# Kernel tuning notes

Measured on AMD Instinct MI355X. Metric: run time of the kernel, lower is better.

The kernel has to match this reference:

```python
import jax, jax.numpy as jnp
import numpy as np

R = 131072          # total proposals (ROIs)
D = 1024            # input feature dim (ShapeSpec.channels)
NUM_CLASSES = 80    # COCO foreground classes
REID_DIM = 256      # reid_feat_dim
BOX_DIM = 4


def setup_inputs() -> dict:
    key = jax.random.key(0)
    ks = jax.random.split(key, 12)
    x = jax.random.normal(ks[0], (R, D), dtype=jnp.float32)
    # cls_score: Linear(D, num_classes+1), init std=0.01, bias 0
    W_cls = 0.01 * jax.random.normal(ks[1], (NUM_CLASSES + 1, D), dtype=jnp.float32)
    b_cls = jnp.zeros((NUM_CLASSES + 1,), dtype=jnp.float32)
    # bbox_pred: Linear(D, num_classes * 4), init std=0.001, bias 0
    W_bbox = 0.001 * jax.random.normal(ks[2], (NUM_CLASSES * BOX_DIM, D), dtype=jnp.float32)
    b_bbox = jnp.zeros((NUM_CLASSES * BOX_DIM,), dtype=jnp.float32)
    # reid_embed_head: MLP(D, 256, 256, 3) -> Linear(D,256), Linear(256,256), Linear(256,256)
    def lin(k, fan_in, fan_out):
        kw, kb = jax.random.split(k)
        bound = 1.0 / np.sqrt(fan_in)
        W = jax.random.uniform(kw, (fan_out, fan_in), minval=-bound, maxval=bound, dtype=jnp.float32)
        b = jax.random.uniform(kb, (fan_out,), minval=-bound, maxval=bound, dtype=jnp.float32)
        return W, b
    W1, b1 = lin(ks[3], D, REID_DIM)
    W2, b2 = lin(ks[4], REID_DIM, REID_DIM)
    W3, b3 = lin(ks[5], REID_DIM, REID_DIM)
    return {"x": x, "W_cls": W_cls, "b_cls": b_cls, "W_bbox": W_bbox, "b_bbox": b_bbox,
            "W1": W1, "b1": b1, "W2": W2, "b2": b2, "W3": W3, "b3": b3}


def reference(x, W_cls, b_cls, W_bbox, b_bbox, W1, b1, W2, b2, W3, b3):
    # x: [R, D] (already flat; torch forward flattens if dim > 2)
    scores = x @ W_cls.T + b_cls                 # [R, K+1]
    proposal_deltas = x @ W_bbox.T + b_bbox      # [R, K*4]
    # MLP with ReLU on all but last layer
    h = jax.nn.relu(x @ W1.T + b1)               # [R, 256]
    h = jax.nn.relu(h @ W2.T + b2)               # [R, 256]
    embeds = h @ W3.T + b3                       # [R, 256]
    return scores, proposal_deltas, embeds
```

## Files before the change

### kernel.cpp

```cpp
#include <hip/hip_runtime.h>
#include <hip/hip_bf16.h>
#include <stdint.h>

#define R_TOT   131072
#define D_IN    1024
#define N_CLS   81
#define N_BOX   320
#define N_H     256
#define N1_USED 657
#define N1_PAD  768
#define NB_COLS 256

typedef __attribute__((ext_vector_type(8))) short short8;
typedef __attribute__((ext_vector_type(4))) float f32x4;

__device__ __forceinline__ unsigned short f2bf(float f) {
  union { float f; unsigned u; } v; v.f = f;
  unsigned r = v.u + 0x7FFFu + ((v.u >> 16) & 1u);
  return (unsigned short)(r >> 16);
}

__device__ __forceinline__ short8 cvt8(float4 a, float4 b) {
  short8 v;
  v[0] = (short)f2bf(a.x); v[1] = (short)f2bf(a.y);
  v[2] = (short)f2bf(a.z); v[3] = (short)f2bf(a.w);
  v[4] = (short)f2bf(b.x); v[5] = (short)f2bf(b.y);
  v[6] = (short)f2bf(b.z); v[7] = (short)f2bf(b.w);
  return v;
}

__device__ __forceinline__ void async_lds16(void* lds, const void* g) {
  __builtin_amdgcn_global_load_lds(
      (const __attribute__((address_space(1))) unsigned int*)g,
      (__attribute__((address_space(3))) unsigned int*)lds, 16, 0, 0);
}

__global__ void prep_w1(const float* __restrict__ Wc, const float* __restrict__ Wb,
                        const float* __restrict__ W1, unsigned short* __restrict__ Wp)
{
  int idx = blockIdx.x * 256 + threadIdx.x;
  int p   = idx / (N1_PAD * 32);
  int rem = idx % (N1_PAD * 32);
  int n   = rem >> 5;
  int kk  = rem & 31;
  int k   = p * 32 + kk;
  float w = 0.f;
  if (n < N_CLS)               w = Wc[(size_t)n * D_IN + k];
  else if (n < N_CLS + N_BOX)  w = Wb[(size_t)(n - N_CLS) * D_IN + k];
  else if (n < N1_USED)        w = W1[(size_t)(n - (N_CLS + N_BOX)) * D_IN + k];
  Wp[idx] = f2bf(w);
}

__global__ void prep_w23(const float* __restrict__ W2, const float* __restrict__ W3,
                         unsigned short* __restrict__ W2b, unsigned short* __restrict__ W3b)
{
  int idx = blockIdx.x * 256 + threadIdx.x;
  if (idx < 65536) W2b[idx] = f2bf(W2[idx]);
  else             W3b[idx - 65536] = f2bf(W3[idx - 65536]);
}

__global__ __launch_bounds__(512) void g1_kernel(
    const float* __restrict__ x, const unsigned short* __restrict__ Wp,
    const float* __restrict__ b_cls, const float* __restrict__ b_box,
    const float* __restrict__ b1,
    float* __restrict__ scores, float* __restrict__ deltas,
    unsigned short* __restrict__ h1)
{
  __shared__ __attribute__((aligned(16))) unsigned short As[64 * 256];

  const int tid  = threadIdx.x;
  const int wave = tid >> 6;
  const int lane = tid & 63;
  const int orig  = blockIdx.x;
  const int work  = (orig & 7) * 768 + (orig >> 3);
  const int m0    = (work / 3) * 64;
  const int nbase = (work % 3) * NB_COLS;

  const int lr  = lane & 15;
  const int hig = lane >> 4;
  const int g2  = hig * 8;

  f32x4 acc[4][2];
#pragma unroll
  for (int i = 0; i < 4; ++i)
#pragma unroll
    for (int j = 0; j < 2; ++j)
      acc[i][j] = (f32x4){0.f, 0.f, 0.f, 0.f};

  const unsigned short* bptr = Wp + (size_t)(nbase + wave * 32 + lr) * 32 + g2;
  const size_t BSTEP = (size_t)N1_PAD * 32;

  short8 bCur0 = *(const short8*)(bptr);
  short8 bCur1 = *(const short8*)(bptr + 512);
  bptr += BSTEP;

#pragma unroll 2
  for (int kp = 0; kp < 32; ++kp) {
    const int kk = kp & 7;

    if (kk == 0) {
      if (kp > 0) __syncthreads();
      const int c0 = (kp >> 3) * 256;
#pragma unroll
      for (int i = 0; i < 4; ++i) {
        int idx = tid + i * 512;
        int row = idx >> 5, s = idx & 31;
        const float* src = x + (size_t)(m0 + row) * D_IN + c0 + s * 8;
        float4 f0 = *(const float4*)src;
        float4 f1 = *(const float4*)(src + 4);
        *(short8*)&As[row * 256 + ((s ^ (row & 7)) << 3)] = cvt8(f0, f1);
      }
      __syncthreads();
    }

    short8 bn0, bn1;
    if (kp < 31) {
      bn0 = *(const short8*)(bptr);
      bn1 = *(const short8*)(bptr + 512);
      bptr += BSTEP;
    }

    const int sb = kk * 4 + hig;
    __builtin_amdgcn_s_setprio(1);
#pragma unroll
    for (int mi = 0; mi < 4; ++mi) {
      const int r  = mi * 16 + lr;
      const int sl = sb ^ (r & 7);
      short8 af = *(const short8*)&As[r * 256 + (sl << 3)];
      acc[mi][0] = __builtin_amdgcn_mfma_f32_16x16x32_bf16(af, bCur0, acc[mi][0], 0, 0, 0);
      acc[mi][1] = __builtin_amdgcn_mfma_f32_16x16x32_bf16(af, bCur1, acc[mi][1], 0, 0, 0);
    }
    __builtin_amdgcn_s_setprio(0);

    if (kp < 31) { bCur0 = bn0; bCur1 = bn1; }
  }

  const int rbase = m0 + (hig << 2);
#pragma unroll
  for (int mi = 0; mi < 4; ++mi) {
#pragma unroll
    for (int ni = 0; ni < 2; ++ni) {
      int n = nbase + wave * 32 + ni * 16 + lr;
      if (n >= N1_USED) continue;
      if (n < N_CLS) {
        float bb = b_cls[n];
#pragma unroll
        for (int j = 0; j < 4; ++j) {
          int r = rbase + mi * 16 + j;
          scores[(size_t)r * N_CLS + n] = acc[mi][ni][j] + bb;
        }
      } else if (n < N_CLS + N_BOX) {
        int nb = n - N_CLS;
        float bb = b_box[nb];
#pragma unroll
        for (int j = 0; j < 4; ++j) {
          int r = rbase + mi * 16 + j;
          deltas[(size_t)r * N_BOX + nb] = acc[mi][ni][j] + bb;
        }
      } else {
        int nh = n - (N_CLS + N_BOX);
        float bb = b1[nh];
#pragma unroll
        for (int j = 0; j < 4; ++j) {
          int r = rbase + mi * 16 + j;
          float h = acc[mi][ni][j] + bb;
          h1[(size_t)r * N_H + nh] = f2bf(fmaxf(h, 0.f));
        }
      }
    }
  }
}

__device__ __forceinline__ void gf_stageA(unsigned short* Asb,
    const unsigned short* __restrict__ A, int m0, int kp, int tid)
{
  int row = tid >> 2, kq = tid & 3;
  async_lds16((char*)Asb + tid * 16,
              (const char*)(A + (size_t)(m0 + row) * N_H + (size_t)kp * 32 + kq * 8));
}
__device__ __forceinline__ void gf_stageB(unsigned short* Bsb,
    const unsigned short* __restrict__ Bw, int kp, int tid)
{
#pragma unroll
  for (int i = 0; i < 2; ++i) {
    int chunk = tid + i * 512;
    int row = chunk >> 2, kq = chunk & 3;
    async_lds16((char*)Bsb + chunk * 16,
                (const char*)(Bw + (size_t)row * N_H + (size_t)kp * 32 + kq * 8));
  }
}

__global__ __launch_bounds__(512, 1) void g23_fused(
    const unsigned short* __restrict__ h1, const unsigned short* __restrict__ W2b,
    const unsigned short* __restrict__ W3b, const float* __restrict__ b2,
    const float* __restrict__ b3, float* __restrict__ embeds)
{
  __shared__ __attribute__((aligned(16))) unsigned short As[2][128 * 32];
  __shared__ __attribute__((aligned(16))) unsigned short Bs[2][256 * 32];
  __shared__ __attribute__((aligned(16))) unsigned short H2[128 * 256];

  const int tid  = threadIdx.x;
  const int wave = tid >> 6, lane = tid & 63;
  const int wm = wave >> 2, wn = wave & 3;
  const int m0 = blockIdx.x * 128;
  const int lr = lane & 15;
  const int hig = lane >> 4;
  const int lk = hig * 8;

  f32x4 acc[4][4];
#pragma unroll
  for (int i = 0; i < 4; ++i)
#pragma unroll
    for (int j = 0; j < 4; ++j)
      acc[i][j] = (f32x4){0.f, 0.f, 0.f, 0.f};

  gf_stageA(&As[0][0], h1, m0, 0, tid);
  gf_stageB(&Bs[0][0], W2b, 0, tid);
  __syncthreads();

  for (int kp = 0; kp < 8; ++kp) {
    const int cur = kp & 1, nxt = cur ^ 1;
    if (kp < 7) { gf_stageA(&As[nxt][0], h1, m0, kp + 1, tid);
                  gf_stageB(&Bs[nxt][0], W2b, kp + 1, tid); }

    short8 af[4], bfr[4];
#pragma unroll
    for (int mi = 0; mi < 4; ++mi)
      af[mi] = *(const short8*)&As[cur][(wm * 64 + mi * 16 + lr) * 32 + lk];
#pragma unroll
    for (int ni = 0; ni < 4; ++ni)
      bfr[ni] = *(const short8*)&Bs[cur][(wn * 64 + ni * 16 + lr) * 32 + lk];
#pragma unroll
    for (int mi = 0; mi < 4; ++mi)
#pragma unroll
      for (int ni = 0; ni < 4; ++ni)
        acc[mi][ni] = __builtin_amdgcn_mfma_f32_16x16x32_bf16(af[mi], bfr[ni], acc[mi][ni], 0, 0, 0);
    __syncthreads();
  }

#pragma unroll
  for (int mi = 0; mi < 4; ++mi) {
#pragma unroll
    for (int ni = 0; ni < 4; ++ni) {
      int n = wn * 64 + ni * 16 + lr;
      float bb = b2[n];
#pragma unroll
      for (int j = 0; j < 4; ++j) {
        int r = wm * 64 + mi * 16 + (hig << 2) + j;
        float v = fmaxf(acc[mi][ni][j] + bb, 0.f);
        H2[r * 256 + (((n >> 3) ^ (r & 7)) << 3) + (n & 7)] = f2bf(v);
      }
      acc[mi][ni] = (f32x4){0.f, 0.f, 0.f, 0.f};
    }
  }
  __syncthreads();

  gf_stageB(&Bs[0][0], W3b, 0, tid);
  __syncthreads();

  for (int kp = 0; kp < 8; ++kp) {
    const int cur = kp & 1, nxt = cur ^ 1;
    if (kp < 7) gf_stageB(&Bs[nxt][0], W3b, kp + 1, tid);

    short8 af[4], bfr[4];
#pragma unroll
    for (int mi = 0; mi < 4; ++mi) {
      const int r  = wm * 64 + mi * 16 + lr;
      const int co = kp * 4 + hig;
      af[mi] = *(const short8*)&H2[r * 256 + ((co ^ (r & 7)) << 3)];
    }
#pragma unroll
    for (int ni = 0; ni < 4; ++ni)
      bfr[ni] = *(const short8*)&Bs[cur][(wn * 64 + ni * 16 + lr) * 32 + lk];
#pragma unroll
    for (int mi = 0; mi < 4; ++mi)
#pragma unroll
      for (int ni = 0; ni < 4; ++ni)
        acc[mi][ni] = __builtin_amdgcn_mfma_f32_16x16x32_bf16(af[mi], bfr[ni], acc[mi][ni], 0, 0, 0);
    __syncthreads();
  }

#pragma unroll
  for (int mi = 0; mi < 4; ++mi) {
#pragma unroll
    for (int ni = 0; ni < 4; ++ni) {
      int n = wn * 64 + ni * 16 + lr;
      float bb = b3[n];
#pragma unroll
      for (int j = 0; j < 4; ++j) {
        int r = m0 + wm * 64 + mi * 16 + (hig << 2) + j;
        embeds[(size_t)r * N_H + n] = acc[mi][ni][j] + bb;
      }
    }
  }
}

extern "C" void kernel_launch(void* const* d_in, const int* in_sizes, int n_in,
                              void* d_out, int out_size, void* d_ws, size_t ws_size,
                              hipStream_t stream)
{
  const float* x     = (const float*)d_in[0];
  const float* W_cls = (const float*)d_in[1];
  const float* b_cls = (const float*)d_in[2];
  const float* W_box = (const float*)d_in[3];
  const float* b_box = (const float*)d_in[4];
  const float* W1    = (const float*)d_in[5];
  const float* b1    = (const float*)d_in[6];
  const float* W2    = (const float*)d_in[7];
  const float* b2    = (const float*)d_in[8];
  const float* W3    = (const float*)d_in[9];
  const float* b3    = (const float*)d_in[10];

  float* scores = (float*)d_out;
  float* deltas = scores + (size_t)R_TOT * N_CLS;
  float* embeds = deltas + (size_t)R_TOT * N_BOX;

  char* ws = (char*)d_ws;
  unsigned short* Wp  = (unsigned short*)ws;
  unsigned short* W2b = (unsigned short*)(ws + 1572864);
  unsigned short* W3b = (unsigned short*)(ws + 1572864 + 131072);
  unsigned short* h1  = (unsigned short*)(ws + 1835008);

  hipLaunchKernelGGL(prep_w1, dim3(3072), dim3(256), 0, stream, W_cls, W_box, W1, Wp);
  hipLaunchKernelGGL(prep_w23, dim3(512), dim3(256), 0, stream, W2, W3, W2b, W3b);
  hipLaunchKernelGGL(g1_kernel, dim3(6144), dim3(512), 0, stream,
                     x, Wp, b_cls, b_box, b1, scores, deltas, h1);
  hipLaunchKernelGGL(g23_fused, dim3(R_TOT / 128), dim3(512), 0, stream,
                     h1, W2b, W3b, b2, b3, embeds);
}
```

Baseline: 425.5 us.

## Enlarge g1 row tile to 128 and switch to 32x32x16 MFMA

The first GEMM kernel now handles 128 rows per block instead of 64, with 8 waves laid out 2x4 so each wave computes a 64x64 tile using 32x32x16 bf16 MFMAs. The aim is to halve the number of times each weight tile is re-read per row and to get more MFMA work out of each LDS and global load. The LDS swizzle widens to 16 and the grid is halved to match. The cost is a larger LDS footprint, more accumulator registers per wave (possibly lower occupancy), and the loss of the previous one-step software prefetch of B fragments.

Measured after the change: 418.6 us. No clear change (-1.6%).

```diff
diff --git a/kernel.cpp b/kernel.cpp
--- a/kernel.cpp
+++ b/kernel.cpp
@@ -11,8 +11,9 @@
 #define N1_PAD  768
 #define NB_COLS 256
 
-typedef __attribute__((ext_vector_type(8))) short short8;
-typedef __attribute__((ext_vector_type(4))) float f32x4;
+typedef __attribute__((ext_vector_type(8)))  short short8;
+typedef __attribute__((ext_vector_type(4)))  float f32x4;
+typedef __attribute__((ext_vector_type(16))) float f32x16;
 
 __device__ __forceinline__ unsigned short f2bf(float f) {
   union { float f; unsigned u; } v; v.f = f;
@@ -26,6 +27,13 @@
   v[2] = (short)f2bf(a.z); v[3] = (short)f2bf(a.w);
   v[4] = (short)f2bf(b.x); v[5] = (short)f2bf(b.y);
   v[6] = (short)f2bf(b.z); v[7] = (short)f2bf(b.w);
+  return v;
+}
+
+__device__ __forceinline__ f32x16 zero16() {
+  f32x16 v;
+#pragma unroll
+  for (int i = 0; i < 16; ++i) v[i] = 0.f;
   return v;
 }
 
@@ -66,104 +74,101 @@
     float* __restrict__ scores, float* __restrict__ deltas,
     unsigned short* __restrict__ h1)
 {
-  __shared__ __attribute__((aligned(16))) unsigned short As[64 * 256];
+  __shared__ __attribute__((aligned(16))) unsigned short As[128 * 256];
 
   const int tid  = threadIdx.x;
   const int wave = tid >> 6;
   const int lane = tid & 63;
   const int orig  = blockIdx.x;
-  const int work  = (orig & 7) * 768 + (orig >> 3);
-  const int m0    = (work / 3) * 64;
+  const int work  = (orig & 7) * 384 + (orig >> 3);
+  const int m0    = (work / 3) * 128;
   const int nbase = (work % 3) * NB_COLS;
 
-  const int lr  = lane & 15;
-  const int hig = lane >> 4;
-  const int g2  = hig * 8;
-
-  f32x4 acc[4][2];
-#pragma unroll
-  for (int i = 0; i < 4; ++i)
-#pragma unroll
-    for (int j = 0; j < 2; ++j)
-      acc[i][j] = (f32x4){0.f, 0.f, 0.f, 0.f};
-
-  const unsigned short* bptr = Wp + (size_t)(nbase + wave * 32 + lr) * 32 + g2;
+  const int wr   = wave >> 2;
+  const int wc   = wave & 3;
+  const int l31  = lane & 31;
+  const int hi32 = lane >> 5;
+
+  f32x16 acc00 = zero16(), acc01 = zero16(), acc10 = zero16(), acc11 = zero16();
+
+  const unsigned short* bptr = Wp + (size_t)(nbase + wc * 64 + l31) * 32 + hi32 * 8;
   const size_t BSTEP = (size_t)N1_PAD * 32;
 
-  short8 bCur0 = *(const short8*)(bptr);
-  short8 bCur1 = *(const short8*)(bptr + 512);
-  bptr += BSTEP;
-
-#pragma unroll 2
   for (int kp = 0; kp < 32; ++kp) {
     const int kk = kp & 7;
 
     if (kk == 0) {
       if (kp > 0) __syncthreads();
       const int c0 = (kp >> 3) * 256;
-#pragma unroll
-      for (int i = 0; i < 4; ++i) {
+#pragma unroll 2
+      for (int i = 0; i < 8; ++i) {
         int idx = tid + i * 512;
         int row = idx >> 5, s = idx & 31;
         const float* src = x + (size_t)(m0 + row) * D_IN + c0 + s * 8;
         float4 f0 = *(const float4*)src;
         float4 f1 = *(const float4*)(src + 4);
-        *(short8*)&As[row * 256 + ((s ^ (row & 7)) << 3)] = cvt8(f0, f1);
+        *(short8*)&As[row * 256 + ((s ^ (row & 15)) << 3)] = cvt8(f0, f1);
       }
       __syncthreads();
     }
 
-    short8 bn0, bn1;
-    if (kp < 31) {
-      bn0 = *(const short8*)(bptr);
-      bn1 = *(const short8*)(bptr + 512);
-      bptr += BSTEP;
-    }
-
-    const int sb = kk * 4 + hig;
+    short8 b0k0 = *(const short8*)(bptr);
+    short8 b0k1 = *(const short8*)(bptr + 16);
+    short8 b1k0 = *(const short8*)(bptr + 1024);
+    short8 b1k1 = *(const short8*)(bptr + 1040);
+    bptr += BSTEP;
+
+    const int kb = kk * 4 + hi32;
+    const int r0 = wr * 64 + l31;
+    const int r1 = r0 + 32;
+    short8 a0k0 = *(const short8*)&As[r0 * 256 + (((kb    ) ^ (r0 & 15)) << 3)];
+    short8 a0k1 = *(const short8*)&As[r0 * 256 + (((kb + 2) ^ (r0 & 15)) << 3)];
+    short8 a1k0 = *(const short8*)&As[r1 * 256 + (((kb    ) ^ (r1 & 15)) << 3)];
+    short8 a1k1 = *(const short8*)&As[r1 * 256 + (((kb + 2) ^ (r1 & 15)) << 3)];
+
     __builtin_amdgcn_s_setprio(1);
-#pragma unroll
-    for (int mi = 0; mi < 4; ++mi) {
-      const int r  = mi * 16 + lr;
-      const int sl = sb ^ (r & 7);
-      short8 af = *(const short8*)&As[r * 256 + (sl << 3)];
-      acc[mi][0] = __builtin_amdgcn_mfma_f32_16x16x32_bf16(af, bCur0, acc[mi][0], 0, 0, 0);
-      acc[mi][1] = __builtin_amdgcn_mfma_f32_16x16x32_bf16(af, bCur1, acc[mi][1], 0, 0, 0);
-    }
+    acc00 = __builtin_amdgcn_mfma_f32_32x32x16_bf16(a0k0, b0k0, acc00, 0, 0, 0);
+    acc01 = __builtin_amdgcn_mfma_f32_32x32x16_bf16(a0k0, b1k0, acc01, 0, 0, 0);
+    acc10 = __builtin_amdgcn_mfma_f32_32x32x16_bf16(a1k0, b0k0, acc10, 0, 0, 0);
+    acc11 = __builtin_amdgcn_mfma_f32_32x32x16_bf16(a1k0, b1k0, acc11, 0, 0, 0);
+    acc00 = __builtin_amdgcn_mfma_f32_32x32x16_bf16(a0k1, b0k1, acc00, 0, 0, 0);
+    acc01 = __builtin_amdgcn_mfma_f32_32x32x16_bf16(a0k1, b1k1, acc01, 0, 0, 0);
+    acc10 = __builtin_amdgcn_mfma_f32_32x32x16_bf16(a1k1, b0k1, acc10, 0, 0, 0);
+    acc11 = __builtin_amdgcn_mfma_f32_32x32x16_bf16(a1k1, b1k1, acc11, 0, 0, 0);
     __builtin_amdgcn_s_setprio(0);
-
-    if (kp < 31) { bCur0 = bn0; bCur1 = bn1; }
-  }
-
-  const int rbase = m0 + (hig << 2);
-#pragma unroll
-  for (int mi = 0; mi < 4; ++mi) {
-#pragma unroll
-    for (int ni = 0; ni < 2; ++ni) {
-      int n = nbase + wave * 32 + ni * 16 + lr;
+  }
+
+#pragma unroll
+  for (int rb = 0; rb < 2; ++rb) {
+#pragma unroll
+    for (int cb = 0; cb < 2; ++cb) {
+      const f32x16 a = (rb == 0) ? (cb == 0 ? acc00 : acc01)
+                                 : (cb == 0 ? acc10 : acc11);
+      const int n = nbase + wc * 64 + cb * 32 + l31;
       if (n >= N1_USED) continue;
+      const int rbase = m0 + wr * 64 + rb * 32 + 4 * hi32;
       if (n < N_CLS) {
         float bb = b_cls[n];
 #pragma unroll
-        for (int j = 0; j < 4; ++j) {
-          int r = rbase + mi * 16 + j;
-          scores[(size_t)r * N_CLS + n] = acc[mi][ni][j] + bb;
+        for (int j = 0; j < 16; ++j) {
+          int r = rbase + (j & 3) + 8 * (j >> 2);
+          scores[(size_t)r * N_CLS + n] = a[j] + bb;
         }
       } else if (n < N_CLS + N_BOX) {
         int nb = n - N_CLS;
         float bb = b_box[nb];
 #pragma unroll
-        for (int j = 0; j < 4; ++j) {
-          int r = rbase + mi * 16 + j;
-          deltas[(size_t)r * N_BOX + nb] = acc[mi][ni][j] + bb;
+        for (int j = 0; j < 16; ++j) {
+          int r = rbase + (j & 3) + 8 * (j >> 2);
+          deltas[(size_t)r * N_BOX + nb] = a[j] + bb;
         }
       } else {
         int nh = n - (N_CLS + N_BOX);
         float bb = b1[nh];
 #pragma unroll
-        for (int j = 0; j < 4; ++j) {
-          int r = rbase + mi * 16 + j;
-          float h = acc[mi][ni][j] + bb;
+        for (int j = 0; j < 16; ++j) {
+          int r = rbase + (j & 3) + 8 * (j >> 2);
+          float h = a[j] + bb;
           h1[(size_t)r * N_H + nh] = f2bf(fmaxf(h, 0.f));
         }
       }
@@ -323,7 +328,7 @@
 
   hipLaunchKernelGGL(prep_w1, dim3(3072), dim3(256), 0, stream, W_cls, W_box, W1, Wp);
   hipLaunchKernelGGL(prep_w23, dim3(512), dim3(256), 0, stream, W2, W3, W2b, W3b);
-  hipLaunchKernelGGL(g1_kernel, dim3(6144), dim3(512), 0, stream,
+  hipLaunchKernelGGL(g1_kernel, dim3(3072), dim3(512), 0, stream,
                      x, Wp, b_cls, b_box, b1, scores, deltas, h1);
   hipLaunchKernelGGL(g23_fused, dim3(R_TOT / 128), dim3(512), 0, stream,
                      h1, W2b, W3b, b2, b3, embeds);
```
